# Performance work log

Hardware: AMD Instinct MI355X
Metric: run time of the kernel (lower is better)

Reference implementation:

```python
import jax, jax.numpy as jnp
import numpy as np

N = 50000      # nodes
E = 500000     # edges
D = 128        # model dim (in_dim == out_dim)
H = 8          # heads
DH = D // H    # head dim = 16
BN_EPS = 1e-5
Z_EPS = 1e-6


def setup_inputs() -> dict:
    key = jax.random.key(0)
    ks = jax.random.split(key, 24)
    w = lambda k, shape, s=0.05: (jax.random.normal(k, shape, jnp.float32) * s)
    inp = {}
    inp['v'] = jax.random.normal(ks[0], (N, D), jnp.float32)
    inp['e'] = jax.random.normal(ks[1], (E, D), jnp.float32)
    inp['envelope'] = jax.random.uniform(ks[2], (E, 1, 1), jnp.float32)
    inp['src'] = jax.random.randint(ks[3], (E,), 0, N, jnp.int32)
    inp['dst'] = jax.random.randint(ks[4], (E,), 0, N, jnp.int32)
    # attention projections (use_bias=False)
    inp['WQ'] = w(ks[5], (D, D)); inp['WK'] = w(ks[6], (D, D))
    inp['WV'] = w(ks[7], (D, D)); inp['We'] = w(ks[8], (D, D))
    # output projections
    inp['WO_v'] = w(ks[9], (D, D)); inp['bO_v'] = jnp.zeros((D,), jnp.float32)
    inp['WO_e'] = w(ks[10], (D, D)); inp['bO_e'] = jnp.zeros((D,), jnp.float32)
    # batch-norm affine params
    inp['g1_v'] = jnp.ones((D,), jnp.float32); inp['b1_v'] = jnp.zeros((D,), jnp.float32)
    inp['g1_e'] = jnp.ones((D,), jnp.float32); inp['b1_e'] = jnp.zeros((D,), jnp.float32)
    inp['g2_v'] = jnp.ones((D,), jnp.float32); inp['b2_v'] = jnp.zeros((D,), jnp.float32)
    inp['g2_e'] = jnp.ones((D,), jnp.float32); inp['b2_e'] = jnp.zeros((D,), jnp.float32)
    # FFN weights (hidden = 2*D)
    inp['W1v'] = w(ks[11], (D, 2 * D)); inp['b1v'] = jnp.zeros((2 * D,), jnp.float32)
    inp['W2v'] = w(ks[12], (2 * D, D)); inp['b2v'] = jnp.zeros((D,), jnp.float32)
    inp['W1e'] = w(ks[13], (D, 2 * D)); inp['b1e'] = jnp.zeros((2 * D,), jnp.float32)
    inp['W2e'] = w(ks[14], (2 * D, D)); inp['b2e'] = jnp.zeros((D,), jnp.float32)
    return inp


def _batchnorm(x, g, b):
    # BatchNorm1d in training mode: biased batch stats over axis 0
    m = x.mean(0)
    var = x.var(0)
    return (x - m) * jax.lax.rsqrt(var + BN_EPS) * g + b


def _forward(v, e, envelope, src, dst,
             WQ, WK, WV, We, WO_v, bO_v, WO_e, bO_e,
             g1_v, b1_v, g1_e, b1_e,
             W1v, b1v, W2v, b2v, W1e, b1e, W2e, b2e,
             g2_v, b2_v, g2_e, b2_e):
    # --- multi-head edge attention ---
    Q = (v @ WQ).reshape(N, H, DH)
    K = (v @ WK).reshape(N, H, DH)
    V = (v @ WV).reshape(N, H, DH)
    pe = (e @ We).reshape(E, H, DH)
    # score = K[src] * Q[dst] / sqrt(Dh) * proj_e   (elementwise, per head)
    score = K[src] * Q[dst] / np.sqrt(DH).astype(np.float32) * pe  # [E,H,Dh]
    e_attn = score.reshape(E, D)                                    # e_out
    s = jnp.exp(jnp.clip(score.sum(-1, keepdims=True), -5.0, 5.0))  # [E,H,1]
    msg = V[src] * envelope * s                                     # [E,H,Dh]
    wV = jax.ops.segment_sum(msg, dst, num_segments=N)              # [N,H,Dh]
    z = jax.ops.segment_sum(s, dst, num_segments=N)                 # [N,H,1]
    v_attn = (wV / (z + Z_EPS)).reshape(N, D)
    # --- O projection + residual + batchnorm ---
    v1 = _batchnorm(v + (v_attn @ WO_v + bO_v), g1_v, b1_v)
    e1 = _batchnorm(e + (e_attn @ WO_e + bO_e), g1_e, b1_e)
    # --- FFN + residual + batchnorm ---
    v2 = _batchnorm(v1 + (jax.nn.relu(v1 @ W1v + b1v) @ W2v + b2v), g2_v, b2_v)
    e2 = _batchnorm(e1 + (jax.nn.relu(e1 @ W1e + b1e) @ W2e + b2e), g2_e, b2_e)
    return v2, e2


def reference(v, e, envelope, src, dst,
              WQ, WK, WV, We, WO_v, bO_v, WO_e, bO_e,
              g1_v, b1_v, g1_e, b1_e,
              W1v, b1v, W2v, b2v, W1e, b1e, W2e, b2e,
              g2_v, b2_v, g2_e, b2_e):
    return _forward(v, e, envelope, src, dst,
                    WQ, WK, WV, We, WO_v, bO_v, WO_e, bO_e,
                    g1_v, b1_v, g1_e, b1_e,
                    W1v, b1v, W2v, b2v, W1e, b1e, W2e, b2e,
                    g2_v, b2_v, g2_e, b2_e)
```

## Files before the change

kernel.cpp:

```cpp
#include <hip/hip_runtime.h>
#include <hip/hip_bf16.h>

#define N_NODES 50000
#define N_EDGES 500000
#define DIM 128
#define RSTRIDE 256

typedef __bf16 bf16_t;
typedef __bf16 bf16x8 __attribute__((ext_vector_type(8)));
typedef __bf16 bf16x2 __attribute__((ext_vector_type(2)));
typedef float f32x4 __attribute__((ext_vector_type(4)));

#define MFMA(a,b,c) __builtin_amdgcn_mfma_f32_16x16x32_bf16((a),(b),(c),0,0,0)

__device__ __forceinline__ int swz(int row, int kbyte){ return kbyte ^ ((row & 7) << 4); }
__device__ __forceinline__ int hswz(int row, int kbyte){ return kbyte ^ ((row & 15) << 4); }

__device__ __forceinline__ bf16x8 lds_frag(const char* s, int row, int rowb, int kbyte){
  return *(const bf16x8*)(s + row * rowb + swz(row, kbyte));
}

__device__ __forceinline__ void copy16(char* dst, const char* __restrict__ src, int bytes){
  for (int o = threadIdx.x * 16; o < bytes; o += blockDim.x * 16)
    *(f32x4*)(dst + o) = *(const f32x4*)(src + o);
}

struct WPrep {
  const float* w[10];
  int Kd[10], Nd[10], off[10], cum[10], mode[10];
};

__global__ void k_wprep(WPrep d, char* img, int total){
  for (int idx = blockIdx.x * blockDim.x + threadIdx.x; idx < total; idx += gridDim.x * blockDim.x){
    int i = 0;
#pragma unroll
    for (int j = 1; j < 10; j++) if (idx >= d.cum[j]) i = j;
    int loc = idx - d.cum[i];
    int K = d.Kd[i], N = d.Nd[i];
    int n = loc / K, k = loc - n * K;
    float val = d.w[i][(size_t)k * N + n];
    int nn = n;
    if (d.mode[i] == 1) nn = ((n & 7) << 4) | (n >> 3);
    if (d.mode[i] == 3) nn = ((n & 15) << 4) | (n >> 4);
    *(bf16_t*)(img + d.off[i] + nn * (K * 2) + swz(nn, k * 2)) = (bf16_t)val;
  }
}

__global__ void k_count(const int* __restrict__ dst, int* __restrict__ cnt){
  int i = blockIdx.x * blockDim.x + threadIdx.x;
  if (i < N_EDGES) atomicAdd(&cnt[dst[i]], 1);
}

__global__ __launch_bounds__(1024) void k_scan(const int* __restrict__ cnt,
                                               int* __restrict__ rowptr, int* __restrict__ wp){
  __shared__ int wsum[16];
  __shared__ int wpre[16];
  __shared__ int scarry;
  const int tid = threadIdx.x, lane = tid & 63, wv = tid >> 6;
  if (tid == 0) scarry = 0;
  for (int base = 0; base < N_NODES; base += 8192){
    int i0 = base + tid * 8;
    int v[8], p[8];
    int tsum = 0;
#pragma unroll
    for (int j = 0; j < 8; j++){
      int idx = i0 + j;
      v[j] = (idx < N_NODES) ? cnt[idx] : 0;
      p[j] = tsum; tsum += v[j];
    }
    int x = tsum;
#pragma unroll
    for (int off = 1; off < 64; off <<= 1){
      int t = __shfl_up(x, off);
      if (lane >= off) x += t;
    }
    if (lane == 63) wsum[wv] = x;
    __syncthreads();
    if (tid == 0){
      int run = scarry;
#pragma unroll
      for (int j = 0; j < 16; j++){ int t = wsum[j]; wpre[j] = run; run += t; }
      scarry = run;
    }
    __syncthreads();
    int texcl = wpre[wv] + x - tsum;
#pragma unroll
    for (int j = 0; j < 8; j++){
      int idx = i0 + j;
      if (idx < N_NODES){ rowptr[idx] = texcl + p[j]; wp[idx] = texcl + p[j]; }
    }
  }
  __syncthreads();
  if (tid == 0) rowptr[N_NODES] = scarry;
}

__global__ void k_fill(const int* __restrict__ dst, int* __restrict__ wp, int* __restrict__ csr){
  int i = blockIdx.x * blockDim.x + threadIdx.x;
  if (i < N_EDGES){
    int p = atomicAdd(&wp[dst[i]], 1);
    csr[p] = i;
  }
}

__global__ __launch_bounds__(512) void k_qkv(
    const float* __restrict__ v, const char* __restrict__ img,
    bf16_t* __restrict__ Q, bf16_t* __restrict__ K, bf16_t* __restrict__ V, int M)
{
  __shared__ __align__(16) char sm[65536];
  char* sX = sm;
  char* sW = sm + 32768;
  const int tid = threadIdx.x, lane = tid & 63, wave = tid >> 6;
  const int r0 = blockIdx.x * 128;
  for (int c = tid; c < 2048; c += 512){
    int row = c >> 4, kc = c & 15, grow = r0 + row;
    float f[8];
    if (grow < M){
      const float4* p = (const float4*)(v + (size_t)grow * DIM + kc * 8);
      float4 u0 = p[0], u1 = p[1];
      f[0]=u0.x; f[1]=u0.y; f[2]=u0.z; f[3]=u0.w;
      f[4]=u1.x; f[5]=u1.y; f[6]=u1.z; f[7]=u1.w;
    } else {
#pragma unroll
      for (int j=0;j<8;j++) f[j] = 0.f;
    }
    bf16x8 o;
#pragma unroll
    for (int j=0;j<8;j++) o[j] = (bf16_t)f[j];
    *(bf16x8*)(sX + row * 256 + swz(row, kc * 16)) = o;
  }
  const int rowA = wave * 16 + (lane & 15);
  const int kb0 = (lane >> 4) * 16;
  const int crow = wave*16 + (lane >> 4)*4;
  const int ccol = lane & 15;
  const f32x4 zero4 = {0.f, 0.f, 0.f, 0.f};
#pragma unroll
  for (int w3 = 0; w3 < 3; w3++){
    __syncthreads();
    copy16(sW, img + w3 * 32768, 32768);
    __syncthreads();
    f32x4 acc[8];
#pragma unroll
    for (int b=0;b<8;b++) acc[b] = zero4;
#pragma unroll
    for (int ks=0; ks<4; ks++){
      bf16x8 a = lds_frag(sX, rowA, 256, ks*64 + kb0);
#pragma unroll
      for (int nt=0; nt<8; nt++){
        int rn = nt*16 + (lane & 15);
        bf16x8 b = lds_frag(sW, rn, 256, ks*64 + kb0);
        acc[nt] = MFMA(a, b, acc[nt]);
      }
    }
    bf16_t* o = (w3 == 0) ? Q : ((w3 == 1) ? K : V);
#pragma unroll
    for (int r=0; r<4; r++){
      int grow = r0 + crow + r;
      if (grow < M){
        bf16x8 t;
#pragma unroll
        for (int nt=0; nt<8; nt++) t[nt] = (bf16_t)acc[nt][r];
        *(bf16x8*)(o + (size_t)grow * DIM + ccol*8) = t;
      }
    }
  }
}

__global__ __launch_bounds__(512, 4) void k_edge(
    const float* __restrict__ e,
    const int* __restrict__ src, const int* __restrict__ dst,
    const bf16_t* __restrict__ Qb, const bf16_t* __restrict__ Kb,
    const char* __restrict__ imgWe, const char* __restrict__ imgWo,
    const float* __restrict__ bOe,
    bf16_t* __restrict__ e1_pre, float* __restrict__ sv,
    float* __restrict__ stats, int M)
{
  __shared__ __align__(16) char sm[66560];
  char* sW = sm;
  char* sX = sm + 32768;
  float* sStats = (float*)(sm + 65536);
  const int tid = threadIdx.x, lane = tid & 63, wave = tid >> 6;
  const int r0 = blockIdx.x * 128;
  const int crow = wave*16 + (lane >> 4)*4;
  const int ccol = lane & 15;
  const int rowA = wave * 16 + (lane & 15);
  const int q = lane >> 4;
  const int kb0 = q * 16;
  bf16x8 Kg[4], Qg[4];
#pragma unroll
  for (int r=0;r<4;r++){
    int ed = r0 + crow + r; if (ed >= M) ed = M - 1;
    int sn = src[ed], dn = dst[ed];
    Kg[r] = *(const bf16x8*)(Kb + (size_t)sn * DIM + ccol * 8);
    Qg[r] = *(const bf16x8*)(Qb + (size_t)dn * DIM + ccol * 8);
  }
  int grA = r0 + rowA; if (grA >= M) grA = M - 1;
  const f32x4* epA = (const f32x4*)(e + (size_t)grA * DIM);
  f32x4 ea[8];
#pragma unroll
  for (int ks=0; ks<4; ks++){
    ea[2*ks]   = epA[ks*8 + q*2];
    ea[2*ks+1] = epA[ks*8 + q*2 + 1];
  }
  copy16(sW, imgWe, 32768);
  if (tid < 256) sStats[tid] = 0.f;
  bf16x8 eAb[4];
#pragma unroll
  for (int ks=0; ks<4; ks++){
#pragma unroll
    for (int j=0;j<4;j++){
      eAb[ks][j]   = (bf16_t)ea[2*ks][j];
      eAb[ks][4+j] = (bf16_t)ea[2*ks+1][j];
    }
  }
  __syncthreads();
  const f32x4 zero4 = {0.f,0.f,0.f,0.f};
  f32x4 wbuf[4];
#pragma unroll
  for (int i=0;i<4;i++) wbuf[i] = *(const f32x4*)(imgWo + tid*16 + i*8192);
  f32x4 pe[8];
#pragma unroll
  for (int i=0;i<8;i++) pe[i] = zero4;
#pragma unroll
  for (int ks=0; ks<4; ks++){
#pragma unroll
    for (int nt=0; nt<8; nt++){
      int rn = nt*16 + (lane & 15);
      bf16x8 b = lds_frag(sW, rn, 256, ks*64 + kb0);
      pe[nt] = MFMA(eAb[ks], b, pe[nt]);
    }
  }
  __syncthreads();
#pragma unroll
  for (int i=0;i<4;i++) *(f32x4*)(sW + tid*16 + i*8192) = wbuf[i];
  f32x4 er[8];
#pragma unroll
  for (int r=0;r<4;r++){
    int gr = r0 + crow + r; if (gr >= M) gr = M - 1;
    const f32x4* rp = (const f32x4*)(e + (size_t)gr*DIM + ccol*8);
    er[2*r]   = rp[0];
    er[2*r+1] = rp[1];
  }
#pragma unroll
  for (int r=0;r<4;r++){
    int row = crow + r;
    bf16x8 t;
    float hsum = 0.f;
#pragma unroll
    for (int nt=0; nt<8; nt++){
      float sc = pe[nt][r] * 0.25f * (float)Kg[r][nt] * (float)Qg[r][nt];
      t[nt] = (bf16_t)sc;
      hsum += sc;
    }
    *(bf16x8*)(sX + row*256 + swz(row, ccol*16)) = t;
    float ts = hsum + __shfl_xor(hsum, 1);
    int ed = r0 + row;
    if (!(ccol & 1) && ed < M)
      sv[(size_t)ed*8 + (ccol >> 1)] = __expf(fminf(5.f, fmaxf(-5.f, ts)));
  }
  __syncthreads();
// ... 100 lines not shown
    bf16_t* __restrict__ v1_pre, float* __restrict__ stats, int M)
{
  __shared__ __align__(16) char sm[66560];
  char* sW = sm;
  char* sX = sm + 32768;
  float* sStats = (float*)(sm + 65536);
  const int tid = threadIdx.x, lane = tid & 63, wave = tid >> 6;
  const int r0 = blockIdx.x * 128;
  copy16(sW, imgWo, 32768);
  if (tid < 256) sStats[tid] = 0.f;
  for (int c = tid; c < 2048; c += 512){
    int row = c >> 4, kc = c & 15, grow = r0 + row;
    bf16x8 o;
    if (grow < M){
      o = *(const bf16x8*)(vAttn + (size_t)grow * DIM + kc * 8);
    } else {
#pragma unroll
      for (int j=0;j<8;j++) o[j] = (bf16_t)0.f;
    }
    *(bf16x8*)(sX + row*256 + swz(row, kc*16)) = o;
  }
  __syncthreads();
  const int rowA = wave*16 + (lane & 15);
  const int kb0 = (lane >> 4)*16;
  const f32x4 zero4 = {0.f,0.f,0.f,0.f};
  f32x4 acc[8];
#pragma unroll
  for (int i=0;i<8;i++) acc[i]=zero4;
#pragma unroll
  for (int ks=0;ks<4;ks++){
    bf16x8 a = lds_frag(sX, rowA, 256, ks*64+kb0);
#pragma unroll
    for (int nt=0;nt<8;nt++){
      int rn = nt*16 + (lane&15);
      bf16x8 b = lds_frag(sW, rn, 256, ks*64+kb0);
      acc[nt] = MFMA(a,b,acc[nt]);
    }
  }
  const int crow = wave*16 + (lane>>4)*4;
  const int ccol = lane & 15;
  float4 bo0 = *(const float4*)(bOv + ccol*8);
  float4 bo1 = *(const float4*)(bOv + ccol*8 + 4);
  float s1[8], s2[8];
#pragma unroll
  for (int j=0;j<8;j++){ s1[j]=0.f; s2[j]=0.f; }
#pragma unroll
  for (int r=0;r<4;r++){
    int grow = r0 + crow + r;
    float val[8];
    if (grow < M){
      const float4* vp = (const float4*)(v + (size_t)grow*DIM + ccol*8);
      float4 v0 = vp[0], v1 = vp[1];
      val[0]=acc[0][r]+v0.x+bo0.x; val[1]=acc[1][r]+v0.y+bo0.y;
      val[2]=acc[2][r]+v0.z+bo0.z; val[3]=acc[3][r]+v0.w+bo0.w;
      val[4]=acc[4][r]+v1.x+bo1.x; val[5]=acc[5][r]+v1.y+bo1.y;
      val[6]=acc[6][r]+v1.z+bo1.z; val[7]=acc[7][r]+v1.w+bo1.w;
      bf16x8 t;
#pragma unroll
      for (int j=0;j<8;j++) t[j] = (bf16_t)val[j];
      *(bf16x8*)(v1_pre + (size_t)grow*RSTRIDE + ccol*8) = t;
    } else {
#pragma unroll
      for (int j=0;j<8;j++) val[j]=0.f;
    }
#pragma unroll
    for (int j=0;j<8;j++){ s1[j] += val[j]; s2[j] += val[j]*val[j]; }
  }
#pragma unroll
  for (int j=0;j<8;j++){
    s1[j] += __shfl_xor(s1[j], 16); s1[j] += __shfl_xor(s1[j], 32);
    s2[j] += __shfl_xor(s2[j], 16); s2[j] += __shfl_xor(s2[j], 32);
  }
  if (lane < 16){
#pragma unroll
    for (int j=0;j<8;j++){
      atomicAdd(&sStats[ccol*8 + j], s1[j]);
      atomicAdd(&sStats[128 + ccol*8 + j], s2[j]);
    }
  }
  __syncthreads();
  if (tid < 256) unsafeAtomicAdd(&stats[tid], sStats[tid]);
}

__global__ __launch_bounds__(512, 4) void k_ffn(
    bf16_t* __restrict__ xio, const float* __restrict__ ss1,
    const char* __restrict__ img1, const float* __restrict__ b1,
    const char* __restrict__ img2, const float* __restrict__ b2,
    float* __restrict__ stats2, int M)
{
  __shared__ __align__(16) char sm[66560];
  char* sA = sm;
  char* sB = sm + 32768;
  float* sStats = (float*)(sm + 65536);
  const int tid = threadIdx.x, lane = tid & 63, wave = tid >> 6;
  const int r0 = blockIdx.x * 128;
  const int rowA = wave*16 + (lane & 15);
  const int q = lane >> 4;
  const int kb0 = q * 16;
  const int crow = wave*16 + q*4;
  const int ccol = lane & 15;
  const f32x4 zero4 = {0.f,0.f,0.f,0.f};

  float4 sc0 = *(const float4*)(ss1 + ccol*8);
  float4 sc1 = *(const float4*)(ss1 + ccol*8 + 4);
  float4 sh0 = *(const float4*)(ss1 + 128 + ccol*8);
  float4 sh1 = *(const float4*)(ss1 + 128 + ccol*8 + 4);
  const float4* bq = (const float4*)(b1 + ccol * 16);
  float4 bq0 = bq[0], bq1 = bq[1], bq2 = bq[2], bq3 = bq[3];

  copy16(sB, img1, 32768);
  if (tid < 256) sStats[tid] = 0.f;
  int grA = r0 + rowA; if (grA >= M) grA = M - 1;
  const bf16_t* xrow = xio + (size_t)grA * RSTRIDE;
  bf16x8 araw[4];
#pragma unroll
  for (int ks=0; ks<4; ks++)
    araw[ks] = *(const bf16x8*)(xrow + ks*32 + q*8);
  bf16x8 xres[4];
#pragma unroll
  for (int r = 0; r < 4; r++){
    int grow = r0 + crow + r;
    bf16x8 o;
    if (grow < M){
      bf16x8 u = *(const bf16x8*)(xio + (size_t)grow*RSTRIDE + ccol*8);
      o[0]=(bf16_t)((float)u[0]*sc0.x+sh0.x); o[1]=(bf16_t)((float)u[1]*sc0.y+sh0.y);
      o[2]=(bf16_t)((float)u[2]*sc0.z+sh0.z); o[3]=(bf16_t)((float)u[3]*sc0.w+sh0.w);
      o[4]=(bf16_t)((float)u[4]*sc1.x+sh1.x); o[5]=(bf16_t)((float)u[5]*sc1.y+sh1.y);
      o[6]=(bf16_t)((float)u[6]*sc1.z+sh1.z); o[7]=(bf16_t)((float)u[7]*sc1.w+sh1.w);
    } else {
#pragma unroll
      for (int j=0;j<8;j++) o[j]=(bf16_t)0.f;
    }
    xres[r] = o;
  }
  bf16x8 xAb[4];
#pragma unroll
  for (int ks=0; ks<4; ks++){
    const f32x4* sp = (const f32x4*)(ss1 + ks*32 + q*8);
    const f32x4* hp = (const f32x4*)(ss1 + 128 + ks*32 + q*8);
    f32x4 s0 = sp[0], s1v = sp[1], h0 = hp[0], h1 = hp[1];
#pragma unroll
    for (int j=0;j<4;j++){
      xAb[ks][j]   = (bf16_t)((float)araw[ks][j]  *s0[j]  + h0[j]);
      xAb[ks][4+j] = (bf16_t)((float)araw[ks][4+j]*s1v[j] + h1[j]);
    }
  }
  __syncthreads();

  bf16x8 hreg[8];
  f32x4 wbuf[4];

#pragma unroll
  for (int i=0;i<4;i++) wbuf[i] = *(const f32x4*)(img1 + 32768 + tid*16 + i*8192);
  {
    f32x4 acc[8];
#pragma unroll
    for (int i=0;i<8;i++) acc[i]=zero4;
#pragma unroll
    for (int ks=0;ks<4;ks++){
#pragma unroll
      for (int nt=0;nt<8;nt++){
        int rn = nt*16 + (lane&15);
        bf16x8 b = lds_frag(sB, rn, 256, ks*64+kb0);
        acc[nt] = MFMA(xAb[ks], b, acc[nt]);
      }
    }
#pragma unroll
    for (int r=0;r<4;r++){
      bf16x8 t;
      t[0]=(bf16_t)fmaxf(acc[0][r]+bq0.x,0.f); t[1]=(bf16_t)fmaxf(acc[1][r]+bq0.y,0.f);
      t[2]=(bf16_t)fmaxf(acc[2][r]+bq0.z,0.f); t[3]=(bf16_t)fmaxf(acc[3][r]+bq0.w,0.f);
      t[4]=(bf16_t)fmaxf(acc[4][r]+bq1.x,0.f); t[5]=(bf16_t)fmaxf(acc[5][r]+bq1.y,0.f);
      t[6]=(bf16_t)fmaxf(acc[6][r]+bq1.z,0.f); t[7]=(bf16_t)fmaxf(acc[7][r]+bq1.w,0.f);
      hreg[r] = t;
    }
  }
  __syncthreads();
#pragma unroll
  for (int i=0;i<4;i++) *(f32x4*)(sB + tid*16 + i*8192) = wbuf[i];
  __syncthreads();
#pragma unroll
  for (int i=0;i<4;i++){
    int o = tid*16 + i*8192;
    wbuf[i] = *(const f32x4*)(img2 + (o >> 8)*512 + (o & 255));
  }
  {
    f32x4 acc[8];
#pragma unroll
    for (int i=0;i<8;i++) acc[i]=zero4;
#pragma unroll
    for (int ks=0;ks<4;ks++){
#pragma unroll
      for (int nt=0;nt<8;nt++){
        int rn = nt*16 + (lane&15);
        bf16x8 b = lds_frag(sB, rn, 256, ks*64+kb0);
        acc[nt] = MFMA(xAb[ks], b, acc[nt]);
      }
    }
#pragma unroll
    for (int r=0;r<4;r++){
      bf16x8 t;
      t[0]=(bf16_t)fmaxf(acc[0][r]+bq2.x,0.f); t[1]=(bf16_t)fmaxf(acc[1][r]+bq2.y,0.f);
      t[2]=(bf16_t)fmaxf(acc[2][r]+bq2.z,0.f); t[3]=(bf16_t)fmaxf(acc[3][r]+bq2.w,0.f);
      t[4]=(bf16_t)fmaxf(acc[4][r]+bq3.x,0.f); t[5]=(bf16_t)fmaxf(acc[5][r]+bq3.y,0.f);
      t[6]=(bf16_t)fmaxf(acc[6][r]+bq3.z,0.f); t[7]=(bf16_t)fmaxf(acc[7][r]+bq3.w,0.f);
      hreg[4+r] = t;
    }
  }
  __syncthreads();

  f32x4 o2[8];
#pragma unroll
  for (int i=0;i<8;i++) o2[i]=zero4;

#pragma unroll
  for (int half = 0; half < 2; half++){
    if ((ccol >> 3) == half){
      int cb = (ccol & 7) * 32;
#pragma unroll
      for (int r=0;r<4;r++){
        int row = crow + r;
        *(bf16x8*)(sA + row*256 + hswz(row, cb))      = hreg[r];
        *(bf16x8*)(sA + row*256 + hswz(row, cb + 16)) = hreg[4+r];
      }
    }
#pragma unroll
    for (int i=0;i<4;i++) *(f32x4*)(sB + tid*16 + i*8192) = wbuf[i];
    __syncthreads();
    if (half == 0){
#pragma unroll
      for (int i=0;i<4;i++){
        int o = tid*16 + i*8192;
        wbuf[i] = *(const f32x4*)(img2 + (o >> 8)*512 + 256 + (o & 255));
      }
    }
#pragma unroll
    for (int ks=0;ks<4;ks++){
      const char* ap = sA + rowA*256 + hswz(rowA, ks*64+kb0);
      bf16x8 a = *(const bf16x8*)ap;
#pragma unroll
      for (int nt=0;nt<8;nt++){
        int rn = nt*16 + (lane&15);
        bf16x8 b = lds_frag(sB, rn, 256, ks*64+kb0);
        o2[nt] = MFMA(a,b,o2[nt]);
      }
    }
    __syncthreads();
  }

  float4 b20 = *(const float4*)(b2 + ccol*8);
  float4 b21 = *(const float4*)(b2 + ccol*8 + 4);
  float s1[8], s2[8];
#pragma unroll
  for (int j=0;j<8;j++){ s1[j]=0.f; s2[j]=0.f; }
#pragma unroll
  for (int r=0;r<4;r++){
    int grow = r0 + crow + r;
    float val[8];
    val[0]=(float)xres[r][0]+o2[0][r]+b20.x; val[1]=(float)xres[r][1]+o2[1][r]+b20.y;
    val[2]=(float)xres[r][2]+o2[2][r]+b20.z; val[3]=(float)xres[r][3]+o2[3][r]+b20.w;
    val[4]=(float)xres[r][4]+o2[4][r]+b21.x; val[5]=(float)xres[r][5]+o2[5][r]+b21.y;
    val[6]=(float)xres[r][6]+o2[6][r]+b21.z; val[7]=(float)xres[r][7]+o2[7][r]+b21.w;
    if (grow < M){
      bf16x8 t;
#pragma unroll
      for (int j=0;j<8;j++) t[j] = (bf16_t)val[j];
      *(bf16x8*)(xio + (size_t)grow*RSTRIDE + ccol*8) = t;
    } else {
#pragma unroll
      for (int j=0;j<8;j++) val[j]=0.f;
    }
#pragma unroll
    for (int j=0;j<8;j++){ s1[j] += val[j]; s2[j] += val[j]*val[j]; }
  }
#pragma unroll
  for (int j=0;j<8;j++){
    s1[j] += __shfl_xor(s1[j], 16); s1[j] += __shfl_xor(s1[j], 32);
    s2[j] += __shfl_xor(s2[j], 16); s2[j] += __shfl_xor(s2[j], 32);
  }
  if (lane < 16){
#pragma unroll
    for (int j=0;j<8;j++){
      atomicAdd(&sStats[ccol*8 + j], s1[j]);
      atomicAdd(&sStats[128 + ccol*8 + j], s2[j]);
    }
  }
  __syncthreads();
  if (tid < 256) unsafeAtomicAdd(&stats2[tid], sStats[tid]);
}

struct FinArgs { const float* st; const float* g; const float* b; float* ss; float invM; };

__global__ void k_finstats(FinArgs a0, FinArgs a1){
  FinArgs a = (blockIdx.x == 0) ? a0 : a1;
  int c = threadIdx.x;
  float mean = a.st[c] * a.invM;
  float var  = a.st[128 + c] * a.invM - mean * mean;
  float scl  = a.g[c] * rsqrtf(var + 1e-5f);
  a.ss[c] = scl;
  a.ss[128 + c] = a.b[c] - mean * scl;
}

__global__ __launch_bounds__(256) void k_norm2(
    char* __restrict__ xv, char* __restrict__ xe,
    const float* __restrict__ ssv, const float* __restrict__ sse,
    long long nv, long long ne)
{
  long long tv = nv * 16, total = tv + ne * 16;
  for (long long g = (long long)blockIdx.x * blockDim.x + threadIdx.x; g < total;
       g += (long long)gridDim.x * blockDim.x){
    bool isv = g < tv;
    char* base = isv ? xv : xe;
    const float* ss = isv ? ssv : sse;
    long long gg = isv ? g : g - tv;
    long long row = gg >> 4;
    int c = (int)(gg & 15);
    bf16x8 u = *(const bf16x8*)(base + row * 512 + c * 16);
    int c0 = c * 8;
    float4 o0, o1;
    o0.x = (float)u[0]*ss[c0+0] + ss[128+c0+0];
    o0.y = (float)u[1]*ss[c0+1] + ss[128+c0+1];
    o0.z = (float)u[2]*ss[c0+2] + ss[128+c0+2];
    o0.w = (float)u[3]*ss[c0+3] + ss[128+c0+3];
    o1.x = (float)u[4]*ss[c0+4] + ss[128+c0+4];
    o1.y = (float)u[5]*ss[c0+5] + ss[128+c0+5];
    o1.z = (float)u[6]*ss[c0+6] + ss[128+c0+6];
    o1.w = (float)u[7]*ss[c0+7] + ss[128+c0+7];
    float4* dp = (float4*)(base + row * 512 + c * 32);
    dp[0] = o0; dp[1] = o1;
  }
}

extern "C" void kernel_launch(void* const* d_in, const int* in_sizes, int n_in,
                              void* d_out, int out_size, void* d_ws, size_t ws_size,
                              hipStream_t stream)
{
  const float* v    = (const float*)d_in[0];
  const float* e    = (const float*)d_in[1];
  const float* envl = (const float*)d_in[2];
  const int*   src  = (const int*)d_in[3];
  const int*   dst  = (const int*)d_in[4];
  const float* bOv  = (const float*)d_in[10];
  const float* bOe  = (const float*)d_in[12];
  const float* g1v  = (const float*)d_in[13];
  const float* b1vn = (const float*)d_in[14];
  const float* g1e  = (const float*)d_in[15];
  const float* b1en = (const float*)d_in[16];
  const float* g2v  = (const float*)d_in[17];
  const float* b2vn = (const float*)d_in[18];
  const float* g2e  = (const float*)d_in[19];
  const float* b2en = (const float*)d_in[20];
  const float* b1vf = (const float*)d_in[22];
  const float* b2vf = (const float*)d_in[24];
  const float* b1ef = (const float*)d_in[26];
  const float* b2ef = (const float*)d_in[28];

  float* out_v = (float*)d_out;
  float* out_e = out_v + (size_t)N_NODES * DIM;
  bf16_t* v1b = (bf16_t*)out_v;
  bf16_t* e1b = (bf16_t*)out_e;

  char* ws = (char*)d_ws;
  const size_t IMG_OFF = 0;
  const size_t QB_OFF  = 458752;
  const size_t KB_OFF  = QB_OFF  + 12800000;
  const size_t VB_OFF  = KB_OFF  + 12800000;
  const size_t VA_OFF  = VB_OFF  + 12800000;
  const size_t SV_OFF  = VA_OFF  + 12800000;
  const size_t CSR_OFF = SV_OFF  + 16000000;
  const size_t RP_OFF  = CSR_OFF + 2000000;
  const size_t WP_OFF  = RP_OFF  + 200016;
  const size_t CNT_OFF = WP_OFF  + 200000;
  const size_t ST_OFF  = CNT_OFF + 200000;
  const size_t SS_OFF  = ST_OFF  + 4096;

  char*   img   = ws + IMG_OFF;
  bf16_t* Qb    = (bf16_t*)(ws + QB_OFF);
  bf16_t* Kb    = (bf16_t*)(ws + KB_OFF);
  bf16_t* Vb    = (bf16_t*)(ws + VB_OFF);
  bf16_t* vAttn = (bf16_t*)(ws + VA_OFF);
  float*  svp   = (float*)(ws + SV_OFF);
  int*    csr   = (int*)(ws + CSR_OFF);
  int*    rowp  = (int*)(ws + RP_OFF);
  int*    wpp   = (int*)(ws + WP_OFF);
  int*    cnt   = (int*)(ws + CNT_OFF);
  float*  st    = (float*)(ws + ST_OFF);
  float*  ssb   = (float*)(ws + SS_OFF);
  float* st_e1 = st;        float* st_v1 = st + 256;
  float* st_v2 = st + 512;  float* st_e2 = st + 768;
  float* ss_v1 = ssb;       float* ss_e1 = ssb + 256;
  float* ss_v2 = ssb + 512; float* ss_e2 = ssb + 768;

  (void)hipMemsetAsync(ws + CNT_OFF, 0, 200000 + 4096, stream);

  WPrep wp;
  const int wid[10]   = {5,6,7,8,9,11,21,23,25,27};
  const int Ks[10]    = {128,128,128,128,128,128,128,256,128,256};
  const int Ns[10]    = {128,128,128,128,128,128,256,128,256,128};
  const int modes[10] = {1,1,1,1,1,1,3,1,3,1};
  int cum = 0, off = 0;
  for (int i = 0; i < 10; i++){
    wp.w[i] = (const float*)d_in[wid[i]];
    wp.Kd[i] = Ks[i]; wp.Nd[i] = Ns[i];
    wp.off[i] = off; wp.cum[i] = cum; wp.mode[i] = modes[i];
    off += Ks[i]*Ns[i]*2; cum += Ks[i]*Ns[i];
  }
  k_wprep<<<896, 256, 0, stream>>>(wp, img, cum);

  k_count<<<1954, 256, 0, stream>>>(dst, cnt);
  k_scan<<<1, 1024, 0, stream>>>(cnt, rowp, wpp);
  k_fill<<<1954, 256, 0, stream>>>(dst, wpp, csr);

  k_qkv<<<391, 512, 0, stream>>>(v, img, Qb, Kb, Vb, N_NODES);

  k_edge<<<3907, 512, 0, stream>>>(e, src, dst, Qb, Kb,
                                   img + 98304 , img + 163840 , bOe,
                                   e1b, svp, st_e1, N_EDGES);

  k_agg<<<6250, 512, 0, stream>>>(rowp, csr, src, envl, svp, Vb, vAttn, N_NODES);

  k_nodeout<<<391, 512, 0, stream>>>(vAttn, v, img + 131072 , bOv,
                                     v1b, st_v1, N_NODES);

  {
    FinArgs fv{st_v1, g1v, b1vn, ss_v1, 1.f / N_NODES};
    FinArgs fe{st_e1, g1e, b1en, ss_e1, 1.f / N_EDGES};
    k_finstats<<<2, 128, 0, stream>>>(fv, fe);
  }

  k_ffn<<<391, 512, 0, stream>>>(v1b, ss_v1, img + 196608 , b1vf,
                                 img + 262144 , b2vf, st_v2, N_NODES);
  k_ffn<<<3907, 512, 0, stream>>>(e1b, ss_e1, img + 327680 , b1ef,
                                  img + 393216 , b2ef, st_e2, N_EDGES);

  {
    FinArgs fv{st_v2, g2v, b2vn, ss_v2, 1.f / N_NODES};
    FinArgs fe{st_e2, g2e, b2en, ss_e2, 1.f / N_EDGES};
    k_finstats<<<2, 128, 0, stream>>>(fv, fe);
  }

  k_norm2<<<4096, 256, 0, stream>>>((char*)out_v, (char*)out_e, ss_v2, ss_e2,
                                    (long long)N_NODES, (long long)N_EDGES);
}
```

Baseline: 723.9 us.

## Merge small kernels into fused launches and fold BN finalization into consumers

Cuts the launch count by merging independent kernels. Weight prep is combined with edge counting, the QKV GEMM with the CSR scan (run by one extra block), and the edge kernel with the CSR fill (extra tail blocks). The node and edge FFN become one launch, and the k_finstats kernels are removed because each FFN and norm block now computes the BN scale and shift into LDS itself. The FFN also preloads both halves of W1 into LDS up front, dropping some syncs. This trades per-block redundant stats math and a single-block scan running alongside the GEMM for fewer launches and less serialization.

```diff
diff --git a/kernel.cpp b/kernel.cpp
--- a/kernel.cpp
+++ b/kernel.cpp
@@ -30,151 +30,151 @@
   int Kd[10], Nd[10], off[10], cum[10], mode[10];
 };
 
-__global__ void k_wprep(WPrep d, char* img, int total){
-  for (int idx = blockIdx.x * blockDim.x + threadIdx.x; idx < total; idx += gridDim.x * blockDim.x){
-    int i = 0;
-#pragma unroll
-    for (int j = 1; j < 10; j++) if (idx >= d.cum[j]) i = j;
-    int loc = idx - d.cum[i];
-    int K = d.Kd[i], N = d.Nd[i];
-    int n = loc / K, k = loc - n * K;
-    float val = d.w[i][(size_t)k * N + n];
-    int nn = n;
-    if (d.mode[i] == 1) nn = ((n & 7) << 4) | (n >> 3);
-    if (d.mode[i] == 3) nn = ((n & 15) << 4) | (n >> 4);
-    *(bf16_t*)(img + d.off[i] + nn * (K * 2) + swz(nn, k * 2)) = (bf16_t)val;
-  }
-}
-
-__global__ void k_count(const int* __restrict__ dst, int* __restrict__ cnt){
-  int i = blockIdx.x * blockDim.x + threadIdx.x;
-  if (i < N_EDGES) atomicAdd(&cnt[dst[i]], 1);
-}
-
-__global__ __launch_bounds__(1024) void k_scan(const int* __restrict__ cnt,
-                                               int* __restrict__ rowptr, int* __restrict__ wp){
-  __shared__ int wsum[16];
-  __shared__ int wpre[16];
-  __shared__ int scarry;
-  const int tid = threadIdx.x, lane = tid & 63, wv = tid >> 6;
-  if (tid == 0) scarry = 0;
-  for (int base = 0; base < N_NODES; base += 8192){
-    int i0 = base + tid * 8;
-    int v[8], p[8];
-    int tsum = 0;
-#pragma unroll
-    for (int j = 0; j < 8; j++){
-      int idx = i0 + j;
-      v[j] = (idx < N_NODES) ? cnt[idx] : 0;
-      p[j] = tsum; tsum += v[j];
-    }
-    int x = tsum;
-#pragma unroll
-    for (int off = 1; off < 64; off <<= 1){
-      int t = __shfl_up(x, off);
-      if (lane >= off) x += t;
-    }
-    if (lane == 63) wsum[wv] = x;
-    __syncthreads();
-    if (tid == 0){
-      int run = scarry;
-#pragma unroll
-      for (int j = 0; j < 16; j++){ int t = wsum[j]; wpre[j] = run; run += t; }
-      scarry = run;
-    }
-    __syncthreads();
-    int texcl = wpre[wv] + x - tsum;
-#pragma unroll
-    for (int j = 0; j < 8; j++){
-      int idx = i0 + j;
-      if (idx < N_NODES){ rowptr[idx] = texcl + p[j]; wp[idx] = texcl + p[j]; }
-    }
-  }
-  __syncthreads();
-  if (tid == 0) rowptr[N_NODES] = scarry;
-}
-
-__global__ void k_fill(const int* __restrict__ dst, int* __restrict__ wp, int* __restrict__ csr){
-  int i = blockIdx.x * blockDim.x + threadIdx.x;
-  if (i < N_EDGES){
-    int p = atomicAdd(&wp[dst[i]], 1);
-    csr[p] = i;
-  }
-}
-
-__global__ __launch_bounds__(512) void k_qkv(
+__global__ __launch_bounds__(512) void k_prep(WPrep d, char* img,
+                                              const int* __restrict__ dst, int* __restrict__ cnt){
+  if (blockIdx.x < 448){
+    int idx = blockIdx.x * 512 + threadIdx.x;
+    if (idx < 229376){
+      int i = 0;
+#pragma unroll
+      for (int j = 1; j < 10; j++) if (idx >= d.cum[j]) i = j;
+      int loc = idx - d.cum[i];
+      int K = d.Kd[i], N = d.Nd[i];
+      int n = loc / K, k = loc - n * K;
+      float val = d.w[i][(size_t)k * N + n];
+      int nn = n;
+      if (d.mode[i] == 1) nn = ((n & 7) << 4) | (n >> 3);
+      if (d.mode[i] == 3) nn = ((n & 15) << 4) | (n >> 4);
+      *(bf16_t*)(img + d.off[i] + nn * (K * 2) + swz(nn, k * 2)) = (bf16_t)val;
+    }
+  } else {
+    int i = (blockIdx.x - 448) * 512 + threadIdx.x;
+    if (i < N_EDGES) atomicAdd(&cnt[dst[i]], 1);
+  }
+}
+
+__global__ __launch_bounds__(512) void k_qkv_scan(
     const float* __restrict__ v, const char* __restrict__ img,
-    bf16_t* __restrict__ Q, bf16_t* __restrict__ K, bf16_t* __restrict__ V, int M)
+    bf16_t* __restrict__ Q, bf16_t* __restrict__ K, bf16_t* __restrict__ V, int M,
+    const int* __restrict__ cnt, int* __restrict__ rowptr, int* __restrict__ wp)
 {
   __shared__ __align__(16) char sm[65536];
-  char* sX = sm;
-  char* sW = sm + 32768;
+  __shared__ int wsum[8], wpre[8], scarry_s;
   const int tid = threadIdx.x, lane = tid & 63, wave = tid >> 6;
-  const int r0 = blockIdx.x * 128;
-  for (int c = tid; c < 2048; c += 512){
-    int row = c >> 4, kc = c & 15, grow = r0 + row;
-    float f[8];
-    if (grow < M){
-      const float4* p = (const float4*)(v + (size_t)grow * DIM + kc * 8);
-      float4 u0 = p[0], u1 = p[1];
-      f[0]=u0.x; f[1]=u0.y; f[2]=u0.z; f[3]=u0.w;
-      f[4]=u1.x; f[5]=u1.y; f[6]=u1.z; f[7]=u1.w;
-    } else {
-#pragma unroll
-      for (int j=0;j<8;j++) f[j] = 0.f;
-    }
-    bf16x8 o;
-#pragma unroll
-    for (int j=0;j<8;j++) o[j] = (bf16_t)f[j];
-    *(bf16x8*)(sX + row * 256 + swz(row, kc * 16)) = o;
-  }
-  const int rowA = wave * 16 + (lane & 15);
-  const int kb0 = (lane >> 4) * 16;
-  const int crow = wave*16 + (lane >> 4)*4;
-  const int ccol = lane & 15;
-  const f32x4 zero4 = {0.f, 0.f, 0.f, 0.f};
-#pragma unroll
-  for (int w3 = 0; w3 < 3; w3++){
-    __syncthreads();
-    copy16(sW, img + w3 * 32768, 32768);
-    __syncthreads();
-    f32x4 acc[8];
-#pragma unroll
-    for (int b=0;b<8;b++) acc[b] = zero4;
-#pragma unroll
-    for (int ks=0; ks<4; ks++){
-      bf16x8 a = lds_frag(sX, rowA, 256, ks*64 + kb0);
-#pragma unroll
-      for (int nt=0; nt<8; nt++){
-        int rn = nt*16 + (lane & 15);
-        bf16x8 b = lds_frag(sW, rn, 256, ks*64 + kb0);
-        acc[nt] = MFMA(a, b, acc[nt]);
+  if (blockIdx.x < 391){
+    char* sX = sm;
+    char* sW = sm + 32768;
+    const int r0 = blockIdx.x * 128;
+    for (int c = tid; c < 2048; c += 512){
+      int row = c >> 4, kc = c & 15, grow = r0 + row;
+      float f[8];
+      if (grow < M){
+        const float4* p = (const float4*)(v + (size_t)grow * DIM + kc * 8);
+        float4 u0 = p[0], u1 = p[1];
+        f[0]=u0.x; f[1]=u0.y; f[2]=u0.z; f[3]=u0.w;
+        f[4]=u1.x; f[5]=u1.y; f[6]=u1.z; f[7]=u1.w;
+      } else {
+#pragma unroll
+        for (int j=0;j<8;j++) f[j] = 0.f;
       }
-    }
-    bf16_t* o = (w3 == 0) ? Q : ((w3 == 1) ? K : V);
-#pragma unroll
-    for (int r=0; r<4; r++){
-      int grow = r0 + crow + r;
-      if (grow < M){
-        bf16x8 t;
-#pragma unroll
-        for (int nt=0; nt<8; nt++) t[nt] = (bf16_t)acc[nt][r];
-        *(bf16x8*)(o + (size_t)grow * DIM + ccol*8) = t;
+      bf16x8 o;
+#pragma unroll
+      for (int j=0;j<8;j++) o[j] = (bf16_t)f[j];
+      *(bf16x8*)(sX + row * 256 + swz(row, kc * 16)) = o;
+    }
+    const int rowA = wave * 16 + (lane & 15);
+    const int kb0 = (lane >> 4) * 16;
+    const int crow = wave*16 + (lane >> 4)*4;
+    const int ccol = lane & 15;
+    const f32x4 zero4 = {0.f, 0.f, 0.f, 0.f};
+#pragma unroll
+    for (int w3 = 0; w3 < 3; w3++){
+      __syncthreads();
+      copy16(sW, img + w3 * 32768, 32768);
+      __syncthreads();
+      f32x4 acc[8];
+#pragma unroll
+      for (int b=0;b<8;b++) acc[b] = zero4;
+#pragma unroll
+      for (int ks=0; ks<4; ks++){
+        bf16x8 a = lds_frag(sX, rowA, 256, ks*64 + kb0);
+#pragma unroll
+        for (int nt=0; nt<8; nt++){
+          int rn = nt*16 + (lane & 15);
+          bf16x8 b = lds_frag(sW, rn, 256, ks*64 + kb0);
+          acc[nt] = MFMA(a, b, acc[nt]);
+        }
       }
-    }
-  }
-}
-
-__global__ __launch_bounds__(512, 4) void k_edge(
+      bf16_t* o = (w3 == 0) ? Q : ((w3 == 1) ? K : V);
+#pragma unroll
+      for (int r=0; r<4; r++){
+        int grow = r0 + crow + r;
+        if (grow < M){
+          bf16x8 t;
+#pragma unroll
+          for (int nt=0; nt<8; nt++) t[nt] = (bf16_t)acc[nt][r];
+          *(bf16x8*)(o + (size_t)grow * DIM + ccol*8) = t;
+        }
+      }
+    }
+  } else {
+    if (tid == 0) scarry_s = 0;
+    for (int base = 0; base < N_NODES; base += 4096){
+      int i0 = base + tid * 8;
+      int vv[8], pp[8];
+      int tsum = 0;
+#pragma unroll
+      for (int j = 0; j < 8; j++){
+        int idx = i0 + j;
+        vv[j] = (idx < N_NODES) ? cnt[idx] : 0;
+        pp[j] = tsum; tsum += vv[j];
+      }
+      int x = tsum;
+#pragma unroll
+      for (int off = 1; off < 64; off <<= 1){
+        int t = __shfl_up(x, off);
+        if (lane >= off) x += t;
+      }
+      if (lane == 63) wsum[wave] = x;
+      __syncthreads();
+      if (tid == 0){
+        int run = scarry_s;
+#pragma unroll
+        for (int j = 0; j < 8; j++){ int t = wsum[j]; wpre[j] = run; run += t; }
+        scarry_s = run;
+      }
+      __syncthreads();
+      int texcl = wpre[wave] + x - tsum;
+#pragma unroll
+      for (int j = 0; j < 8; j++){
+        int idx = i0 + j;
+        if (idx < N_NODES){ rowptr[idx] = texcl + pp[j]; wp[idx] = texcl + pp[j]; }
+      }
+      __syncthreads();
+    }
+    if (tid == 0) rowptr[N_NODES] = scarry_s;
+  }
+}
+
+__global__ __launch_bounds__(512, 4) void k_edge_fill(
     const float* __restrict__ e,
     const int* __restrict__ src, const int* __restrict__ dst,
     const bf16_t* __restrict__ Qb, const bf16_t* __restrict__ Kb,
     const char* __restrict__ imgWe, const char* __restrict__ imgWo,
     const float* __restrict__ bOe,
     bf16_t* __restrict__ e1_pre, float* __restrict__ sv,
-    float* __restrict__ stats, int M)
+    float* __restrict__ stats, int M,
+    int* __restrict__ wpF, int* __restrict__ csrF)
 {
   __shared__ __align__(16) char sm[66560];
+  if (blockIdx.x >= 3907){
+    int i = (blockIdx.x - 3907) * 512 + threadIdx.x;
+    if (i < N_EDGES){
+      int pp = atomicAdd(&wpF[dst[i]], 1);
+      csrF[pp] = i;
+    }
+    return;
+  }
   char* sW = sm;
   char* sX = sm + 32768;
   float* sStats = (float*)(sm + 65536);
@@ -441,18 +441,23 @@
   if (tid < 256) unsafeAtomicAdd(&stats[tid], sStats[tid]);
 }
 
-__global__ __launch_bounds__(512, 4) void k_ffn(
-    bf16_t* __restrict__ xio, const float* __restrict__ ss1,
-    const char* __restrict__ img1, const float* __restrict__ b1,
-    const char* __restrict__ img2, const float* __restrict__ b2,
-    float* __restrict__ stats2, int M)
-{
-  __shared__ __align__(16) char sm[66560];
+struct FfnP {
+  bf16_t* xio; const float* st; const float* g; const float* bn;
+  const char* img1; const float* b1; const char* img2; const float* b2;
+  float* stats2; int M; float invM;
+};
+
+__global__ __launch_bounds__(512, 4) void k_ffn(FfnP pv, FfnP pe, int nv){
+  __shared__ __align__(16) char sm[67584];
   char* sA = sm;
   char* sB = sm + 32768;
   float* sStats = (float*)(sm + 65536);
+  float* sSS    = (float*)(sm + 66560);
+  FfnP p; int bid;
+  if ((int)blockIdx.x < nv){ p = pv; bid = blockIdx.x; }
+  else { p = pe; bid = blockIdx.x - nv; }
   const int tid = threadIdx.x, lane = tid & 63, wave = tid >> 6;
-  const int r0 = blockIdx.x * 128;
+  const int r0 = bid * 128;
   const int rowA = wave*16 + (lane & 15);
   const int q = lane >> 4;
   const int kb0 = q * 16;
@@ -460,57 +465,72 @@
   const int ccol = lane & 15;
   const f32x4 zero4 = {0.f,0.f,0.f,0.f};
 
-  float4 sc0 = *(const float4*)(ss1 + ccol*8);
-  float4 sc1 = *(const float4*)(ss1 + ccol*8 + 4);
-  float4 sh0 = *(const float4*)(ss1 + 128 + ccol*8);
-  float4 sh1 = *(const float4*)(ss1 + 128 + ccol*8 + 4);
-  const float4* bq = (const float4*)(b1 + ccol * 16);
-  float4 bq0 = bq[0], bq1 = bq[1], bq2 = bq[2], bq3 = bq[3];
-
-  copy16(sB, img1, 32768);
+  if (tid < 128){
+    float mean = p.st[tid] * p.invM;
+    float var  = p.st[128 + tid] * p.invM - mean * mean;
+    float scl  = p.g[tid] * rsqrtf(var + 1e-5f);
+    sSS[tid] = scl;
+    sSS[128 + tid] = p.bn[tid] - mean * scl;
+  }
   if (tid < 256) sStats[tid] = 0.f;
-  int grA = r0 + rowA; if (grA >= M) grA = M - 1;
-  const bf16_t* xrow = xio + (size_t)grA * RSTRIDE;
+  copy16(sB, p.img1, 32768);
+  copy16(sA, p.img1 + 32768, 32768);
+  int grA = r0 + rowA; if (grA >= p.M) grA = p.M - 1;
+  const bf16_t* xrow = p.xio + (size_t)grA * RSTRIDE;
   bf16x8 araw[4];
 #pragma unroll
   for (int ks=0; ks<4; ks++)
     araw[ks] = *(const bf16x8*)(xrow + ks*32 + q*8);
-  bf16x8 xres[4];
+  bf16x8 ufoot[4];
 #pragma unroll
   for (int r = 0; r < 4; r++){
     int grow = r0 + crow + r;
+    if (grow < p.M) ufoot[r] = *(const bf16x8*)(p.xio + (size_t)grow*RSTRIDE + ccol*8);
+    else {
+#pragma unroll
+      for (int j=0;j<8;j++) ufoot[r][j] = (bf16_t)0.f;
+    }
+  }
+  const float4* bqp = (const float4*)(p.b1 + ccol * 16);
+  float4 bq0 = bqp[0], bq1 = bqp[1], bq2 = bqp[2], bq3 = bqp[3];
+  __syncthreads();
+
+  f32x4 scA0 = *(const f32x4*)(sSS + ccol*8);
+  f32x4 scA1 = *(const f32x4*)(sSS + ccol*8 + 4);
+  f32x4 shA0 = *(const f32x4*)(sSS + 128 + ccol*8);
+  f32x4 shA1 = *(const f32x4*)(sSS + 128 + ccol*8 + 4);
+  bf16x8 xres[4];
+#pragma unroll
+  for (int r = 0; r < 4; r++){
     bf16x8 o;
-    if (grow < M){
-      bf16x8 u = *(const bf16x8*)(xio + (size_t)grow*RSTRIDE + ccol*8);
-      o[0]=(bf16_t)((float)u[0]*sc0.x+sh0.x); o[1]=(bf16_t)((float)u[1]*sc0.y+sh0.y);
-      o[2]=(bf16_t)((float)u[2]*sc0.z+sh0.z); o[3]=(bf16_t)((float)u[3]*sc0.w+sh0.w);
-      o[4]=(bf16_t)((float)u[4]*sc1.x+sh1.x); o[5]=(bf16_t)((float)u[5]*sc1.y+sh1.y);
-      o[6]=(bf16_t)((float)u[6]*sc1.z+sh1.z); o[7]=(bf16_t)((float)u[7]*sc1.w+sh1.w);
-    } else {
-#pragma unroll
-      for (int j=0;j<8;j++) o[j]=(bf16_t)0.f;
+#pragma unroll
+    for (int j=0;j<4;j++){
+      o[j]   = (bf16_t)((float)ufoot[r][j]  *scA0[j] + shA0[j]);
+      o[4+j] = (bf16_t)((float)ufoot[r][4+j]*scA1[j] + shA1[j]);
     }
     xres[r] = o;
   }
   bf16x8 xAb[4];
 #pragma unroll
   for (int ks=0; ks<4; ks++){
-    const f32x4* sp = (const f32x4*)(ss1 + ks*32 + q*8);
-    const f32x4* hp = (const f32x4*)(ss1 + 128 + ks*32 + q*8);
-    f32x4 s0 = sp[0], s1v = sp[1], h0 = hp[0], h1 = hp[1];
+    f32x4 s0 = *(const f32x4*)(sSS + ks*32 + q*8);
+    f32x4 s1v = *(const f32x4*)(sSS + ks*32 + q*8 + 4);
+    f32x4 h0 = *(const f32x4*)(sSS + 128 + ks*32 + q*8);
+    f32x4 h1 = *(const f32x4*)(sSS + 128 + ks*32 + q*8 + 4);
 #pragma unroll
     for (int j=0;j<4;j++){
       xAb[ks][j]   = (bf16_t)((float)araw[ks][j]  *s0[j]  + h0[j]);
       xAb[ks][4+j] = (bf16_t)((float)araw[ks][4+j]*s1v[j] + h1[j]);
     }
   }
-  __syncthreads();
+  f32x4 wbuf[4];
+#pragma unroll
+  for (int i=0;i<4;i++){
+    int o = tid*16 + i*8192;
+    wbuf[i] = *(const f32x4*)(p.img2 + (o >> 8)*512 + (o & 255));
+  }
 
   bf16x8 hreg[8];
-  f32x4 wbuf[4];
-
-#pragma unroll
-  for (int i=0;i<4;i++) wbuf[i] = *(const f32x4*)(img1 + 32768 + tid*16 + i*8192);
   {
     f32x4 acc[8];
 #pragma unroll
@@ -534,15 +554,6 @@
       hreg[r] = t;
     }
   }
-  __syncthreads();
-#pragma unroll
-  for (int i=0;i<4;i++) *(f32x4*)(sB + tid*16 + i*8192) = wbuf[i];
-  __syncthreads();
-#pragma unroll
-  for (int i=0;i<4;i++){
-    int o = tid*16 + i*8192;
-    wbuf[i] = *(const f32x4*)(img2 + (o >> 8)*512 + (o & 255));
-  }
   {
     f32x4 acc[8];
 #pragma unroll
@@ -552,7 +563,7 @@
 #pragma unroll
       for (int nt=0;nt<8;nt++){
         int rn = nt*16 + (lane&15);
-        bf16x8 b = lds_frag(sB, rn, 256, ks*64+kb0);
+        bf16x8 b = lds_frag(sA, rn, 256, ks*64+kb0);
         acc[nt] = MFMA(xAb[ks], b, acc[nt]);
       }
     }
@@ -568,47 +579,63 @@
   }
   __syncthreads();
 
+  if ((ccol >> 3) == 0){
+    int cb = (ccol & 7) * 32;
+#pragma unroll
+    for (int r=0;r<4;r++){
+      int row = crow + r;
+      *(bf16x8*)(sA + row*256 + hswz(row, cb))      = hreg[r];
+      *(bf16x8*)(sA + row*256 + hswz(row, cb + 16)) = hreg[4+r];
+    }
+  }
+#pragma unroll
+  for (int i=0;i<4;i++) *(f32x4*)(sB + tid*16 + i*8192) = wbuf[i];
+  __syncthreads();
+
+#pragma unroll
+  for (int i=0;i<4;i++){
+    int o = tid*16 + i*8192;
+    wbuf[i] = *(const f32x4*)(p.img2 + (o >> 8)*512 + 256 + (o & 255));
+  }
   f32x4 o2[8];
 #pragma unroll
   for (int i=0;i<8;i++) o2[i]=zero4;
-
-#pragma unroll
-  for (int half = 0; half < 2; half++){
-    if ((ccol >> 3) == half){
-      int cb = (ccol & 7) * 32;
-#pragma unroll
-      for (int r=0;r<4;r++){
-        int row = crow + r;
-        *(bf16x8*)(sA + row*256 + hswz(row, cb))      = hreg[r];
-        *(bf16x8*)(sA + row*256 + hswz(row, cb + 16)) = hreg[4+r];
-      }
-    }
-#pragma unroll
-    for (int i=0;i<4;i++) *(f32x4*)(sB + tid*16 + i*8192) = wbuf[i];
-    __syncthreads();
-    if (half == 0){
-#pragma unroll
-      for (int i=0;i<4;i++){
-        int o = tid*16 + i*8192;
-        wbuf[i] = *(const f32x4*)(img2 + (o >> 8)*512 + 256 + (o & 255));
-      }
-    }
-#pragma unroll
-    for (int ks=0;ks<4;ks++){
-      const char* ap = sA + rowA*256 + hswz(rowA, ks*64+kb0);
-      bf16x8 a = *(const bf16x8*)ap;
-#pragma unroll
-      for (int nt=0;nt<8;nt++){
-        int rn = nt*16 + (lane&15);
-        bf16x8 b = lds_frag(sB, rn, 256, ks*64+kb0);
-        o2[nt] = MFMA(a,b,o2[nt]);
-      }
-    }
-    __syncthreads();
-  }
-
-  float4 b20 = *(const float4*)(b2 + ccol*8);
-  float4 b21 = *(const float4*)(b2 + ccol*8 + 4);
+#pragma unroll
+  for (int ks=0;ks<4;ks++){
+    bf16x8 a = *(const bf16x8*)(sA + rowA*256 + hswz(rowA, ks*64+kb0));
+#pragma unroll
+    for (int nt=0;nt<8;nt++){
+      int rn = nt*16 + (lane&15);
+      bf16x8 b = lds_frag(sB, rn, 256, ks*64+kb0);
+      o2[nt] = MFMA(a,b,o2[nt]);
+    }
+  }
+  __syncthreads();
+  if ((ccol >> 3) == 1){
+    int cb = (ccol & 7) * 32;
+#pragma unroll
+    for (int r=0;r<4;r++){
+      int row = crow + r;
+      *(bf16x8*)(sA + row*256 + hswz(row, cb))      = hreg[r];
+      *(bf16x8*)(sA + row*256 + hswz(row, cb + 16)) = hreg[4+r];
+    }
+  }
+#pragma unroll
+  for (int i=0;i<4;i++) *(f32x4*)(sB + tid*16 + i*8192) = wbuf[i];
+  __syncthreads();
+  float4 b20 = *(const float4*)(p.b2 + ccol*8);
+  float4 b21 = *(const float4*)(p.b2 + ccol*8 + 4);
+#pragma unroll
+  for (int ks=0;ks<4;ks++){
+    bf16x8 a = *(const bf16x8*)(sA + rowA*256 + hswz(rowA, ks*64+kb0));
+#pragma unroll
+    for (int nt=0;nt<8;nt++){
+      int rn = nt*16 + (lane&15);
+      bf16x8 b = lds_frag(sB, rn, 256, ks*64+kb0);
+      o2[nt] = MFMA(a,b,o2[nt]);
+    }
+  }
+
   float s1[8], s2[8];
 #pragma unroll
   for (int j=0;j<8;j++){ s1[j]=0.f; s2[j]=0.f; }
@@ -620,11 +647,11 @@
     val[2]=(float)xres[r][2]+o2[2][r]+b20.z; val[3]=(float)xres[r][3]+o2[3][r]+b20.w;
     val[4]=(float)xres[r][4]+o2[4][r]+b21.x; val[5]=(float)xres[r][5]+o2[5][r]+b21.y;
     val[6]=(float)xres[r][6]+o2[6][r]+b21.z; val[7]=(float)xres[r][7]+o2[7][r]+b21.w;
-    if (grow < M){
+    if (grow < p.M){
       bf16x8 t;
 #pragma unroll
       for (int j=0;j<8;j++) t[j] = (bf16_t)val[j];
-      *(bf16x8*)(xio + (size_t)grow*RSTRIDE + ccol*8) = t;
+      *(bf16x8*)(p.xio + (size_t)grow*RSTRIDE + ccol*8) = t;
     } else {
 #pragma unroll
       for (int j=0;j<8;j++) val[j]=0.f;
@@ -645,32 +672,33 @@
     }
   }
   __syncthreads();
-  if (tid < 256) unsafeAtomicAdd(&stats2[tid], sStats[tid]);
-}
-
-struct FinArgs { const float* st; const float* g; const float* b; float* ss; float invM; };
-
-__global__ void k_finstats(FinArgs a0, FinArgs a1){
-  FinArgs a = (blockIdx.x == 0) ? a0 : a1;
-  int c = threadIdx.x;
-  float mean = a.st[c] * a.invM;
-  float var  = a.st[128 + c] * a.invM - mean * mean;
-  float scl  = a.g[c] * rsqrtf(var + 1e-5f);
-  a.ss[c] = scl;
-  a.ss[128 + c] = a.b[c] - mean * scl;
-}
+  if (tid < 256) unsafeAtomicAdd(&p.stats2[tid], sStats[tid]);
+}
+
+struct NormP { const float* st; const float* g; const float* bn; float invM; };
 
 __global__ __launch_bounds__(256) void k_norm2(
     char* __restrict__ xv, char* __restrict__ xe,
-    const float* __restrict__ ssv, const float* __restrict__ sse,
-    long long nv, long long ne)
+    NormP pv, NormP pe, long long nv, long long ne)
 {
+  __shared__ float sSS[512];
+  const int tid = threadIdx.x;
+  {
+    int side = tid >> 7, c = tid & 127;
+    NormP pp = side ? pe : pv;
+    float mean = pp.st[c] * pp.invM;
+    float var  = pp.st[128 + c] * pp.invM - mean * mean;
+    float scl  = pp.g[c] * rsqrtf(var + 1e-5f);
+    sSS[side*256 + c] = scl;
+    sSS[side*256 + 128 + c] = pp.bn[c] - mean * scl;
+  }
+  __syncthreads();
   long long tv = nv * 16, total = tv + ne * 16;
-  for (long long g = (long long)blockIdx.x * blockDim.x + threadIdx.x; g < total;
+  for (long long g = (long long)blockIdx.x * blockDim.x + tid; g < total;
        g += (long long)gridDim.x * blockDim.x){
     bool isv = g < tv;
     char* base = isv ? xv : xe;
-    const float* ss = isv ? ssv : sse;
+    const float* ss = isv ? sSS : (sSS + 256);
     long long gg = isv ? g : g - tv;
     long long row = gg >> 4;
     int c = (int)(gg & 15);
@@ -731,7 +759,6 @@
   const size_t WP_OFF  = RP_OFF  + 200016;
   const size_t CNT_OFF = WP_OFF  + 200000;
   const size_t ST_OFF  = CNT_OFF + 200000;
-  const size_t SS_OFF  = ST_OFF  + 4096;
 
   char*   img   = ws + IMG_OFF;
   bf16_t* Qb    = (bf16_t*)(ws + QB_OFF);
@@ -744,11 +771,8 @@
   int*    wpp   = (int*)(ws + WP_OFF);
   int*    cnt   = (int*)(ws + CNT_OFF);
   float*  st    = (float*)(ws + ST_OFF);
-  float*  ssb   = (float*)(ws + SS_OFF);
   float* st_e1 = st;        float* st_v1 = st + 256;
   float* st_v2 = st + 512;  float* st_e2 = st + 768;
-  float* ss_v1 = ssb;       float* ss_e1 = ssb + 256;
-  float* ss_v2 = ssb + 512; float* ss_e2 = ssb + 768;
 
   (void)hipMemsetAsync(ws + CNT_OFF, 0, 200000 + 4096, stream);
 
@@ -764,40 +788,22 @@
     wp.off[i] = off; wp.cum[i] = cum; wp.mode[i] = modes[i];
     off += Ks[i]*Ns[i]*2; cum += Ks[i]*Ns[i];
   }
-  k_wprep<<<896, 256, 0, stream>>>(wp, img, cum);
-
-  k_count<<<1954, 256, 0, stream>>>(dst, cnt);
-  k_scan<<<1, 1024, 0, stream>>>(cnt, rowp, wpp);
-  k_fill<<<1954, 256, 0, stream>>>(dst, wpp, csr);
-
-  k_qkv<<<391, 512, 0, stream>>>(v, img, Qb, Kb, Vb, N_NODES);
-
-  k_edge<<<3907, 512, 0, stream>>>(e, src, dst, Qb, Kb,
-                                   img + 98304 , img + 163840 , bOe,
-                                   e1b, svp, st_e1, N_EDGES);
-
+
+  k_prep<<<1425, 512, 0, stream>>>(wp, img, dst, cnt);
+  k_qkv_scan<<<392, 512, 0, stream>>>(v, img, Qb, Kb, Vb, N_NODES, cnt, rowp, wpp);
+  k_edge_fill<<<4884, 512, 0, stream>>>(e, src, dst, Qb, Kb,
+                                        img + 98304 , img + 163840 , bOe,
+                                        e1b, svp, st_e1, N_EDGES, wpp, csr);
   k_agg<<<6250, 512, 0, stream>>>(rowp, csr, src, envl, svp, Vb, vAttn, N_NODES);
-
   k_nodeout<<<391, 512, 0, stream>>>(vAttn, v, img + 131072 , bOv,
                                      v1b, st_v1, N_NODES);
-
-  {
-    FinArgs fv{st_v1, g1v, b1vn, ss_v1, 1.f / N_NODES};
-    FinArgs fe{st_e1, g1e, b1en, ss_e1, 1.f / N_EDGES};
-    k_finstats<<<2, 128, 0, stream>>>(fv, fe);
-  }
-
-  k_ffn<<<391, 512, 0, stream>>>(v1b, ss_v1, img + 196608 , b1vf,
-                                 img + 262144 , b2vf, st_v2, N_NODES);
-  k_ffn<<<3907, 512, 0, stream>>>(e1b, ss_e1, img + 327680 , b1ef,
-                                  img + 393216 , b2ef, st_e2, N_EDGES);
-
-  {
-    FinArgs fv{st_v2, g2v, b2vn, ss_v2, 1.f / N_NODES};
-    FinArgs fe{st_e2, g2e, b2en, ss_e2, 1.f / N_EDGES};
-    k_finstats<<<2, 128, 0, stream>>>(fv, fe);
-  }
-
-  k_norm2<<<4096, 256, 0, stream>>>((char*)out_v, (char*)out_e, ss_v2, ss_e2,
+  FfnP pv{v1b, st_v1, g1v, b1vn, img + 196608, b1vf, img + 262144, b2vf,
+          st_v2, N_NODES, 1.f / N_NODES};
+  FfnP pe{e1b, st_e1, g1e, b1en, img + 327680, b1ef, img + 393216, b2ef,
+          st_e2, N_EDGES, 1.f / N_EDGES};
+  k_ffn<<<4298, 512, 0, stream>>>(pv, pe, 391);
+  NormP npv{st_v2, g2v, b2vn, 1.f / N_NODES};
+  NormP npe{st_e2, g2e, b2en, 1.f / N_EDGES};
+  k_norm2<<<4096, 256, 0, stream>>>((char*)out_v, (char*)out_e, npv, npe,
                                     (long long)N_NODES, (long long)N_EDGES);
 }
```

Result: slower. 828.3 us (+14.4%).
